# Kernel optimization log

Measured on AMD Instinct MI355X. Metric: run time of the kernel, lower is better.

## Reference

```python
import jax, jax.numpy as jnp
import numpy as np


def setup_inputs() -> dict:
    key = jax.random.key(0)
    k1, k2, k3, k4, k5 = jax.random.split(key, 5)
    N, M = 8192, 8192
    ref_kpts = jax.random.normal(k1, (N, 3), dtype=jnp.float32)
    src_kpts = jax.random.normal(k2, (M, 3), dtype=jnp.float32)
    gt_transform = jax.random.normal(k3, (4, 4), dtype=jnp.float32)
    ref_sigma = jax.random.uniform(k4, (N,), dtype=jnp.float32)
    src_sigma = jax.random.uniform(k5, (M,), dtype=jnp.float32)
    return {"ref_kpts": ref_kpts, "src_kpts": src_kpts, "gt_transform": gt_transform,
            "ref_sigma": ref_sigma, "src_sigma": src_sigma}


def reference(ref_kpts, src_kpts, gt_transform, ref_sigma, src_sigma):
    # apply_transform: rigid SE(3): p @ R^T + t
    R = gt_transform[:3, :3]
    t = gt_transform[:3, 3]
    kpts2 = src_kpts @ R.T + t  # [M, 3]
    # pairwise euclidean distances [N, M]
    diff = jnp.linalg.norm(ref_kpts[:, None, :] - kpts2[None, :, :], axis=-1)
    # forward direction: for each ref point, nearest transformed src point
    min_dist_fwd = jnp.min(diff, axis=-1)        # [N]
    idx_fwd = jnp.argmin(diff, axis=-1)          # [N]
    sigma_fwd = (ref_sigma + src_sigma[idx_fwd]) * 0.5
    forward_loss = jnp.mean(jnp.log(sigma_fwd) + min_dist_fwd / sigma_fwd)
    # backward direction: for each src point, nearest ref point
    min_dist_bwd = jnp.min(diff, axis=0)         # [M]
    idx_bwd = jnp.argmin(diff, axis=0)           # [M]
    sigma_bwd = (src_sigma + ref_sigma[idx_bwd]) * 0.5
    backward_loss = jnp.mean(jnp.log(sigma_bwd) + min_dist_bwd / sigma_bwd)
    return forward_loss + backward_loss
```

## Files before the change

kernel.cpp:

```cpp
#include <hip/hip_runtime.h>
#include <math.h>

typedef float v2f __attribute__((ext_vector_type(2)));
typedef float v4f __attribute__((ext_vector_type(4)));

#define TPB 256
#define IPT 4
#define JS  128


__global__ __launch_bounds__(256) void setup_kernel(
    const float* __restrict__ ref, const float* __restrict__ src,
    const float* __restrict__ T,
    float* __restrict__ refI, float* __restrict__ srcI,
    unsigned long long* __restrict__ packF,
    unsigned long long* __restrict__ packB,
    float* __restrict__ out, int N, int M) {
  int i = blockIdx.x * blockDim.x + threadIdx.x;
  if (i < M) {
    float x = src[3 * i], y = src[3 * i + 1], z = src[3 * i + 2];
    float tx = T[0] * x + T[1] * y + T[2]  * z + T[3];
    float ty = T[4] * x + T[5] * y + T[6]  * z + T[7];
    float tz = T[8] * x + T[9] * y + T[10] * z + T[11];
    int base = 8 * (i >> 1) + (i & 1);
    srcI[base]     = tx;
    srcI[base + 2] = ty;
    srcI[base + 4] = tz;
    srcI[base + 6] = tx * tx + ty * ty + tz * tz;
    packB[i] = ~0ull;
  }
  if (i < N) {
    float x = ref[3 * i], y = ref[3 * i + 1], z = ref[3 * i + 2];
    int base = 8 * (i >> 1) + (i & 1);
    refI[base]     = x;
    refI[base + 2] = y;
    refI[base + 4] = z;
    refI[base + 6] = x * x + y * y + z * z;
    packF[i] = ~0ull;
  }
  if (i == 0) {
    out[0] = 0.0f;
#pragma unroll
    for (int e = 0; e < 2; e++) {
      int bn = 8 * ((N + e) >> 1) + ((N + e) & 1);
      refI[bn] = 0.f; refI[bn + 2] = 0.f; refI[bn + 4] = 0.f;
      refI[bn + 6] = INFINITY;
      int bm = 8 * ((M + e) >> 1) + ((M + e) & 1);
      srcI[bm] = 0.f; srcI[bm + 2] = 0.f; srcI[bm + 4] = 0.f;
      srcI[bm + 6] = INFINITY;
    }
  }
}

__device__ __forceinline__ unsigned int sortable(float f) {
  unsigned int u = __float_as_uint(f);
  return u ^ ((unsigned int)((int)u >> 31) | 0x80000000u);
}

__global__ __launch_bounds__(TPB, 4) void pairs_kernel(
    const float* __restrict__ refI, const float* __restrict__ srcI,
    unsigned long long* __restrict__ packF,
    unsigned long long* __restrict__ packB,
    int N, int M, int nbF) {
  int b = blockIdx.x;
  const float *selfI, *otherI;
  unsigned long long* pack;
  int selfN, otherN;
  if (b < nbF) {
    selfI = refI; otherI = srcI; pack = packF; selfN = N; otherN = M;
  } else {
    b -= nbF;
    selfI = srcI; otherI = refI; pack = packB; selfN = M; otherN = N;
  }
  const int ib = b / JS, jb = b % JS;
  const int i0 = ib * (TPB * IPT) + threadIdx.x;

  float ax[IPT], ay[IPT], az[IPT], mind[IPT];
  int mini[IPT];
#pragma unroll
  for (int k = 0; k < IPT; k++) {
    int i = i0 + k * TPB;
    int ic = (i < selfN) ? i : (selfN - 1);
    int base = 8 * (ic >> 1) + (ic & 1);
    ax[k] = -2.0f * selfI[base];
    ay[k] = -2.0f * selfI[base + 2];
    az[k] = -2.0f * selfI[base + 4];
    mind[k] = INFINITY; mini[k] = 0;
  }

  int chunk = (otherN + JS - 1) / JS;
  chunk = (chunk + 1) & ~1;
  const int j0 = jb * chunk;
  const int jcount = min(chunk, otherN - j0);

  const v4f* og = (const v4f*)(otherI + 4 * j0);

#pragma unroll 4
  for (int jj = 0; jj < jcount; jj += 2) {
    v4f A = og[jj];
    v4f B = og[jj + 1];
    v2f qx = __builtin_shufflevector(A, A, 0, 1);
    v2f qy = __builtin_shufflevector(A, A, 2, 3);
    v2f qz = __builtin_shufflevector(B, B, 0, 1);
    v2f qw = __builtin_shufflevector(B, B, 2, 3);
#pragma unroll
    for (int k = 0; k < IPT; k++) {
      v2f t = __builtin_elementwise_fma((v2f){ax[k], ax[k]}, qx, qw);
      t = __builtin_elementwise_fma((v2f){ay[k], ay[k]}, qy, t);
      t = __builtin_elementwise_fma((v2f){az[k], az[k]}, qz, t);
      if (t.x < mind[k]) { mind[k] = t.x; mini[k] = jj; }
      if (t.y < mind[k]) { mind[k] = t.y; mini[k] = jj + 1; }
    }
  }

#pragma unroll
  for (int k = 0; k < IPT; k++) {
    int i = i0 + k * TPB;
    if (i < selfN && jcount > 0) {
      unsigned long long p = ((unsigned long long)sortable(mind[k]) << 32) |
                             (unsigned int)(j0 + mini[k]);
      atomicMin(&pack[i], p);
    }
  }
}

__global__ __launch_bounds__(256) void finalize_kernel(
    const unsigned long long* __restrict__ packF,
    const unsigned long long* __restrict__ packB,
    const float* __restrict__ refI, const float* __restrict__ srcI,
    const float* __restrict__ ref_sigma, const float* __restrict__ src_sigma,
    float* __restrict__ out, int N, int M) {
  int gid = blockIdx.x * blockDim.x + threadIdx.x;
  float term = 0.f;
  if (gid < N) {
    int idx = (int)(packF[gid] & 0xffffffffu);
    int sb = 8 * (gid >> 1) + (gid & 1);
    int ob = 8 * (idx >> 1) + (idx & 1);
    float dx = refI[sb]     - srcI[ob];
    float dy = refI[sb + 2] - srcI[ob + 2];
    float dz = refI[sb + 4] - srcI[ob + 4];
    float d = sqrtf(dx * dx + dy * dy + dz * dz);
    float sigma = 0.5f * (ref_sigma[gid] + src_sigma[idx]);
    term = (logf(sigma) + d / sigma) * (1.0f / (float)N);
  } else if (gid < N + M) {
    int j = gid - N;
    int idx = (int)(packB[j] & 0xffffffffu);
    int sb = 8 * (j >> 1) + (j & 1);
    int ob = 8 * (idx >> 1) + (idx & 1);
    float dx = srcI[sb]     - refI[ob];
    float dy = srcI[sb + 2] - refI[ob + 2];
    float dz = srcI[sb + 4] - refI[ob + 4];
    float d = sqrtf(dx * dx + dy * dy + dz * dz);
    float sigma = 0.5f * (src_sigma[j] + ref_sigma[idx]);
    term = (logf(sigma) + d / sigma) * (1.0f / (float)M);
  }
#pragma unroll
  for (int o = 32; o > 0; o >>= 1) term += __shfl_down(term, o, 64);
  __shared__ float wsum[4];
  const int lane = threadIdx.x & 63, wid = threadIdx.x >> 6;
  if (lane == 0) wsum[wid] = term;
  __syncthreads();
  if (threadIdx.x == 0)
    atomicAdd(out, wsum[0] + wsum[1] + wsum[2] + wsum[3]);
}

extern "C" void kernel_launch(void* const* d_in, const int* in_sizes, int n_in,
                              void* d_out, int out_size, void* d_ws,
                              size_t ws_size, hipStream_t stream) {
  const float* ref_kpts  = (const float*)d_in[0];
  const float* src_kpts  = (const float*)d_in[1];
  const float* gt        = (const float*)d_in[2];
  const float* ref_sigma = (const float*)d_in[3];
  const float* src_sigma = (const float*)d_in[4];
  float* out = (float*)d_out;

  const int N = in_sizes[0] / 3;
  const int M = in_sizes[1] / 3;

  const int NG8 = 8 * ((N + 3) / 2);
  const int MG8 = 8 * ((M + 3) / 2);
  float* f = (float*)d_ws;
  float* refI = f;
  float* srcI = f + NG8;
  unsigned long long* packF = (unsigned long long*)(f + NG8 + MG8);
  unsigned long long* packB = packF + N;

  int nPts = (N > M) ? N : M;
  setup_kernel<<<(nPts + 255) / 256, 256, 0, stream>>>(
      ref_kpts, src_kpts, gt, refI, srcI, packF, packB, out, N, M);

  const int ibF = (N + TPB * IPT - 1) / (TPB * IPT);
  const int ibB = (M + TPB * IPT - 1) / (TPB * IPT);
  const int nbF = ibF * JS;
  const int nbB = ibB * JS;
  pairs_kernel<<<nbF + nbB, TPB, 0, stream>>>(refI, srcI, packF, packB,
                                              N, M, nbF);

  finalize_kernel<<<(N + M + 255) / 256, 256, 0, stream>>>(
      packF, packB, refI, srcI, ref_sigma, src_sigma, out, N, M);
}
```

Measured before the change: 87.98 us.

## Pack argmin index into float mantissa bits and double points per thread

```diff
diff --git a/kernel.cpp b/kernel.cpp
--- a/kernel.cpp
+++ b/kernel.cpp
@@ -1,11 +1,10 @@
 #include <hip/hip_runtime.h>
 #include <math.h>
 
-typedef float v2f __attribute__((ext_vector_type(2)));
 typedef float v4f __attribute__((ext_vector_type(4)));
 
 #define TPB 256
-#define IPT 4
+#define IPT 8
 #define JS  128
 
 
@@ -44,10 +43,10 @@
     for (int e = 0; e < 2; e++) {
       int bn = 8 * ((N + e) >> 1) + ((N + e) & 1);
       refI[bn] = 0.f; refI[bn + 2] = 0.f; refI[bn + 4] = 0.f;
-      refI[bn + 6] = INFINITY;
+      refI[bn + 6] = 1e30f;
       int bm = 8 * ((M + e) >> 1) + ((M + e) & 1);
       srcI[bm] = 0.f; srcI[bm + 2] = 0.f; srcI[bm + 4] = 0.f;
-      srcI[bm + 6] = INFINITY;
+      srcI[bm + 6] = 1e30f;
     }
   }
 }
@@ -75,8 +74,7 @@
   const int ib = b / JS, jb = b % JS;
   const int i0 = ib * (TPB * IPT) + threadIdx.x;
 
-  float ax[IPT], ay[IPT], az[IPT], mind[IPT];
-  int mini[IPT];
+  float ax[IPT], ay[IPT], az[IPT], m0[IPT], m1[IPT];
 #pragma unroll
   for (int k = 0; k < IPT; k++) {
     int i = i0 + k * TPB;
@@ -85,7 +83,7 @@
     ax[k] = -2.0f * selfI[base];
     ay[k] = -2.0f * selfI[base + 2];
     az[k] = -2.0f * selfI[base + 4];
-    mind[k] = INFINITY; mini[k] = 0;
+    m0[k] = 1e30f; m1[k] = 1e30f;
   }
 
   int chunk = (otherN + JS - 1) / JS;
@@ -93,23 +91,28 @@
   const int j0 = jb * chunk;
   const int jcount = min(chunk, otherN - j0);
 
+  const int lowbits = 32 - __clz((chunk > 2 ? chunk : 2) - 1);
+  const unsigned keep = ~((1u << lowbits) - 1u);
+
   const v4f* og = (const v4f*)(otherI + 4 * j0);
 
-#pragma unroll 4
+#pragma unroll 2
   for (int jj = 0; jj < jcount; jj += 2) {
     v4f A = og[jj];
     v4f B = og[jj + 1];
-    v2f qx = __builtin_shufflevector(A, A, 0, 1);
-    v2f qy = __builtin_shufflevector(A, A, 2, 3);
-    v2f qz = __builtin_shufflevector(B, B, 0, 1);
-    v2f qw = __builtin_shufflevector(B, B, 2, 3);
 #pragma unroll
     for (int k = 0; k < IPT; k++) {
-      v2f t = __builtin_elementwise_fma((v2f){ax[k], ax[k]}, qx, qw);
-      t = __builtin_elementwise_fma((v2f){ay[k], ay[k]}, qy, t);
-      t = __builtin_elementwise_fma((v2f){az[k], az[k]}, qz, t);
-      if (t.x < mind[k]) { mind[k] = t.x; mini[k] = jj; }
-      if (t.y < mind[k]) { mind[k] = t.y; mini[k] = jj + 1; }
+      float u0 = __builtin_fmaf(ax[k], A.x, B.z);
+      u0 = __builtin_fmaf(ay[k], A.z, u0);
+      u0 = __builtin_fmaf(az[k], B.x, u0);
+      float u1 = __builtin_fmaf(ax[k], A.y, B.w);
+      u1 = __builtin_fmaf(ay[k], A.w, u1);
+      u1 = __builtin_fmaf(az[k], B.y, u1);
+      float e0 = __uint_as_float((__float_as_uint(u0) & keep) | (unsigned)jj);
+      float e1 = __uint_as_float((__float_as_uint(u1) & keep) |
+                                 (unsigned)(jj + 1));
+      m0[k] = fminf(m0[k], e0);
+      m1[k] = fminf(m1[k], e1);
     }
   }
 
@@ -117,8 +120,11 @@
   for (int k = 0; k < IPT; k++) {
     int i = i0 + k * TPB;
     if (i < selfN && jcount > 0) {
-      unsigned long long p = ((unsigned long long)sortable(mind[k]) << 32) |
-                             (unsigned int)(j0 + mini[k]);
+      float mf = fminf(m0[k], m1[k]);
+      unsigned mb = __float_as_uint(mf);
+      int jloc = (int)(mb & ~keep);
+      unsigned long long p = ((unsigned long long)sortable(mf) << 32) |
+                             (unsigned int)(j0 + jloc);
       atomicMin(&pack[i], p);
     }
   }
```

After: 90.27 us. +2.6%, slower.
